# Kernel optimization log

Hardware: AMD Instinct MI355X
Metric: run time of the kernel (lower is better)

Reference implementation:

```python
import jax, jax.numpy as jnp
import numpy as np

B, M, V, E, D, T = 512, 64, 20000, 1024, 384, 100
EPS = 1e-5


def setup_inputs() -> dict:
    key = jax.random.key(0)
    ks = jax.random.split(key, 26)
    w = lambda k, shape: (jax.random.normal(k, shape, jnp.float32) * 0.02)
    return {
        'x': jax.random.uniform(ks[0], (B, V), jnp.float32),
        'emb': jax.random.normal(ks[1], (B, M, D), jnp.float32),
        'lengths': jax.random.randint(ks[2], (B,), 1, M + 1, jnp.int32),
        'fc11_w': w(ks[3], (E, V)), 'fc11_b': jnp.zeros((E,), jnp.float32),
        'fc12_w': w(ks[4], (E, E)), 'fc12_b': jnp.zeros((E,), jnp.float32),
        'q_w': w(ks[5], (D, E)), 'q_b': jnp.zeros((D,), jnp.float32),
        'k_w': w(ks[6], (D, D)), 'k_b': jnp.zeros((D,), jnp.float32),
        'v_w': w(ks[7], (D, D)), 'v_b': jnp.zeros((D,), jnp.float32),
        'mean_w': w(ks[8], (T, D)), 'mean_b': jnp.zeros((T,), jnp.float32),
        'logvar_w': w(ks[9], (T, D)), 'logvar_b': jnp.zeros((T,), jnp.float32),
        'mean_bn_b': jnp.zeros((T,), jnp.float32),
        'logvar_bn_b': jnp.zeros((T,), jnp.float32),
        'dec_w': w(ks[10], (V, T)), 'dec_b': jnp.zeros((V,), jnp.float32),
        'dec_bn_b': jnp.zeros((V,), jnp.float32),
    }


def _bn(h, bias):
    # BatchNorm1d, training-mode batch stats, weight frozen at 1 (requires_grad=False)
    mu = h.mean(axis=0)
    var = h.var(axis=0)  # biased variance, as torch BN normalization
    return (h - mu) / jnp.sqrt(var + EPS) + bias


def reference(x, emb, lengths, fc11_w, fc11_b, fc12_w, fc12_b,
              q_w, q_b, k_w, k_b, v_w, v_b,
              mean_w, mean_b, logvar_w, logvar_b,
              mean_bn_b, logvar_bn_b, dec_w, dec_b, dec_bn_b):
    # encoder MLP (dropout p=0 -> identity)
    e1 = jax.nn.softplus(x @ fc11_w.T + fc11_b)
    h_bow = jax.nn.softplus(e1 @ fc12_w.T + fc12_b)  # [B, E]

    # ragged single-query attention over sentence embeddings, vectorized
    q = h_bow @ q_w.T + q_b                              # [B, D]
    k = jnp.einsum('bmd,ed->bme', emb, k_w) + k_b        # [B, M, D]
    v = jnp.einsum('bmd,ed->bme', emb, v_w) + v_b        # [B, M, D]
    scores = jnp.einsum('bd,bmd->bm', q, k) / jnp.sqrt(jnp.float32(D))
    valid = jnp.arange(M)[None, :] < lengths[:, None]    # [B, M]
    scores = jnp.where(valid, scores, -jnp.inf)
    alpha = jax.nn.softmax(scores, axis=-1)
    d_i = jnp.einsum('bm,bmd->bd', alpha, v)             # [B, D]

    mu = _bn(d_i @ mean_w.T + mean_b, mean_bn_b)         # [B, T]
    logvar = _bn(d_i @ logvar_w.T + logvar_b, logvar_bn_b)
    z = mu  # eval-mode reparameterize
    theta = jax.nn.softmax(z, axis=1)

    logit = theta @ dec_w.T + dec_b
    recon_log = jax.nn.log_softmax(_bn(logit, dec_bn_b), axis=-1)
    recon_loss = -(x * recon_log).sum(axis=1).mean()

    # KL prior: a = ones -> mu2 = 0, var2 = 1 - 1/T (scalar)
    var2 = 1.0 - 1.0 / T
    var = jnp.exp(logvar)
    kld = 0.5 * ((var / var2 + mu * mu / var2 + jnp.log(var2) - logvar).sum(axis=1) - T)
    loss_kl = kld.mean()
    return recon_loss + loss_kl
```

## Files before the change

kernel.cpp:

```cpp
#include <hip/hip_runtime.h>
#include <cstddef>

#define NB 512
#define NM 64
#define NV 20000
#define NE 1024
#define ND 384
#define NT 100
#define EPS 1e-5f

#define NVP 20096
#define NKP 128
#define NHS 256

typedef __bf16 bf16x8 __attribute__((ext_vector_type(8)));
typedef float f32x4 __attribute__((ext_vector_type(4)));

__device__ __forceinline__ float softplus_f(float x) {
    return fmaxf(x, 0.f) + log1pf(expf(-fabsf(x)));
}

__device__ __forceinline__ unsigned short f2bf(float f) {
    unsigned u = __builtin_bit_cast(unsigned, f);
    unsigned r = u + 0x7FFFu + ((u >> 16) & 1u);
    return (unsigned short)(r >> 16);
}

__device__ __forceinline__ float bf2f(unsigned short u) {
    return __builtin_bit_cast(float, (unsigned)u << 16);
}

__device__ __forceinline__ uint4 pack_bf8(float4 a, float4 b) {
    bf16x8 v;
    v[0] = (__bf16)a.x; v[1] = (__bf16)a.y; v[2] = (__bf16)a.z; v[3] = (__bf16)a.w;
    v[4] = (__bf16)b.x; v[5] = (__bf16)b.y; v[6] = (__bf16)b.z; v[7] = (__bf16)b.w;
    return __builtin_bit_cast(uint4, v);
}

__device__ __forceinline__ void convert8(const float* __restrict__ s,
                                         unsigned short* __restrict__ d,
                                         int b, int tid) {
    const size_t i = ((size_t)b * 256 + tid) * 8;
    const float4 a = *reinterpret_cast<const float4*>(s + i);
    const float4 c = *reinterpret_cast<const float4*>(s + i + 4);
    *reinterpret_cast<uint4*>(d + i) = pack_bf8(a, c);
}

#define PREP_C12 512
#define PREP_QW  192
#define PREP_VW  72
#define PREP_TR  144
#define PREP_HD  257
#define PREP_DW  (NVP / 2)
#define PREP_BLOCKS (PREP_C12 + PREP_QW + PREP_VW + PREP_TR + PREP_HD + PREP_DW)

__global__ __launch_bounds__(256) void prep_kernel(
        const float* __restrict__ fc12_w, unsigned short* __restrict__ w12b,
        const float* __restrict__ q_w,    unsigned short* __restrict__ qwb,
        const float* __restrict__ v_w,    unsigned short* __restrict__ vwb,
        const float* __restrict__ k_w,    unsigned short* __restrict__ kTb,
        const float* __restrict__ mw, const float* __restrict__ lw,
        const float* __restrict__ mb, const float* __restrict__ lb,
        unsigned short* __restrict__ headwb, float* __restrict__ headbb,
        const float* __restrict__ dec_w,  unsigned short* __restrict__ decwb) {
    __shared__ float tile[32][33];
    int b = blockIdx.x;
    const int tid = threadIdx.x;
    if (b < PREP_C12) { convert8(fc12_w, w12b, b, tid); return; }
    b -= PREP_C12;
    if (b < PREP_QW) { convert8(q_w, qwb, b, tid); return; }
    b -= PREP_QW;
    if (b < PREP_VW) { convert8(v_w, vwb, b, tid); return; }
    b -= PREP_VW;
    if (b < PREP_TR) {
        const int bx = (b % 12) * 32, by = (b / 12) * 32;
        const int tx = tid & 31, ty = tid >> 5;
        #pragma unroll
        for (int i = 0; i < 4; ++i)
            tile[ty + 8 * i][tx] = k_w[(size_t)(by + ty + 8 * i) * ND + bx + tx];
        __syncthreads();
        #pragma unroll
        for (int i = 0; i < 4; ++i)
            kTb[(size_t)(bx + ty + 8 * i) * ND + by + tx] = f2bf(tile[tx][ty + 8 * i]);
        return;
    }
    b -= PREP_TR;
    if (b < PREP_HD) {
        if (b == NHS) {
            if (tid < NHS)
                headbb[tid] = (tid < NT) ? mb[tid]
                            : (tid >= 128 && tid < 128 + NT) ? lb[tid - 128] : 0.f;
            return;
        }
        const float* src = (b < NT) ? (mw + (size_t)b * ND)
                         : (b >= 128 && b < 128 + NT) ? (lw + (size_t)(b - 128) * ND) : nullptr;
        for (int c = tid; c < ND; c += 256)
            headwb[(size_t)b * ND + c] = src ? f2bf(src[c]) : (unsigned short)0;
        return;
    }
    b -= PREP_HD;
    {
        const int n = b * 2 + (tid >> 7);
        const int k = tid & 127;
        decwb[(size_t)n * NKP + k] =
            (n < NV && k < NT) ? f2bf(dec_w[(size_t)n * NT + k]) : (unsigned short)0;
    }
}

#define BM 128
#define BN 128
#define BK 32

__device__ __forceinline__ int lds_off(int row, int slot) {
    return row * BK + ((slot ^ ((row >> 1) & 3)) << 3);
}

__global__ __launch_bounds__(512, 2) void gemm_f32_256(
        const float* __restrict__ A,
        const float* __restrict__ Bw,
        unsigned short* __restrict__ partial,
        int M, int N, int K, int S, int steps_total) {
    __shared__ __align__(16) unsigned short Asl[256 * BK];
    __shared__ __align__(16) unsigned short Bsl[256 * BK];
    const int tid = threadIdx.x;
    const int xcd = blockIdx.x & 7;
    const int l = blockIdx.x >> 3;
    const int tile = l & 7;
    const int s = xcd + 8 * (l >> 3);
    const int bm = tile & 1, bn = tile >> 1;
    const int row0 = bm * 256, col0 = bn * 256;
    const int k_begin = (int)(((long)s * steps_total) / S) * BK;
    const int k_end   = (int)(((long)(s + 1) * steps_total) / S) * BK;
    const int nsteps = (k_end - k_begin) / BK;

    const int sr = tid >> 1;
    const int sc = (tid & 1) * 16;
    const int sslot = (tid & 1) * 2;
    const int wave = tid >> 6, lane = tid & 63;
    const int wm = wave >> 2, wn = wave & 3;
    const int lrow = lane & 15, lkb = lane >> 4;

    f32x4 acc[8][4] = {};
    const float* Ab = A + (size_t)row0 * K;
    const float* Bb = Bw + (size_t)col0 * K;

    float4 ra[4], rb[4];

#define LOADREGS(K0)                                                          \
    {                                                                         \
        const float* pa = Ab + (size_t)sr * K + (K0) + sc;                    \
        const float* pb = Bb + (size_t)sr * K + (K0) + sc;                    \
        ra[0] = *reinterpret_cast<const float4*>(pa);                         \
        ra[1] = *reinterpret_cast<const float4*>(pa + 4);                     \
        ra[2] = *reinterpret_cast<const float4*>(pa + 8);                     \
        ra[3] = *reinterpret_cast<const float4*>(pa + 12);                    \
        rb[0] = *reinterpret_cast<const float4*>(pb);                         \
        rb[1] = *reinterpret_cast<const float4*>(pb + 4);                     \
        rb[2] = *reinterpret_cast<const float4*>(pb + 8);                     \
        rb[3] = *reinterpret_cast<const float4*>(pb + 12);                    \
    }

#define WRITELDS()                                                            \
    {                                                                         \
        *reinterpret_cast<uint4*>(&Asl[lds_off(sr, sslot)])     = pack_bf8(ra[0], ra[1]); \
        *reinterpret_cast<uint4*>(&Asl[lds_off(sr, sslot + 1)]) = pack_bf8(ra[2], ra[3]); \
        *reinterpret_cast<uint4*>(&Bsl[lds_off(sr, sslot)])     = pack_bf8(rb[0], rb[1]); \
        *reinterpret_cast<uint4*>(&Bsl[lds_off(sr, sslot + 1)]) = pack_bf8(rb[2], rb[3]); \
    }

    LOADREGS(k_begin);
    WRITELDS();
    __syncthreads();

    for (int t = 0; t < nsteps; ++t) {
        const bool has_next = (t + 1) < nsteps;
        if (has_next) LOADREGS(k_begin + (t + 1) * BK);

        bf16x8 af[8], bfr[4];
        #pragma unroll
        for (int i = 0; i < 8; ++i)
            af[i] = *reinterpret_cast<const bf16x8*>(&Asl[lds_off(wm * 128 + i * 16 + lrow, lkb)]);
        #pragma unroll
        for (int j = 0; j < 4; ++j)
            bfr[j] = *reinterpret_cast<const bf16x8*>(&Bsl[lds_off(wn * 64 + j * 16 + lrow, lkb)]);
        #pragma unroll
        for (int i = 0; i < 8; ++i)
            #pragma unroll
            for (int j = 0; j < 4; ++j)
                acc[i][j] = __builtin_amdgcn_mfma_f32_16x16x32_bf16(af[i], bfr[j], acc[i][j], 0, 0, 0);

        __syncthreads();
        if (has_next) WRITELDS();
        __syncthreads();
    }
#undef LOADREGS
#undef WRITELDS

    unsigned short* P = partial + (size_t)s * M * N;
    #pragma unroll
    for (int i = 0; i < 8; ++i) {
        const int rbase = row0 + wm * 128 + i * 16 + lkb * 4;
        #pragma unroll
        for (int j = 0; j < 4; ++j) {
            const int col = col0 + wn * 64 + j * 16 + lrow;
            #pragma unroll
            for (int r = 0; r < 4; ++r)
                P[(size_t)(rbase + r) * N + col] = f2bf(acc[i][j][r]);
        }
    }
}

__global__ __launch_bounds__(256) void gemm_mfma_splitk(
        const unsigned short* __restrict__ A,
        const unsigned short* __restrict__ Bw,
        unsigned short* __restrict__ partial,
        int M, int N, int K, int S, int steps_total) {
    __shared__ __align__(16) unsigned short Asl[BM * BK];
    __shared__ __align__(16) unsigned short Bsl[BN * BK];
    const int tid = threadIdx.x;
    const int bn = blockIdx.x, bm = blockIdx.y, s = blockIdx.z;
    const int row0 = bm * BM, col0 = bn * BN;
    const int k_begin = (int)(((long)s * steps_total) / S) * BK;
    const int k_end   = (int)(((long)(s + 1) * steps_total) / S) * BK;

    const int srow = tid >> 2;
    const int scol = (tid & 3) * 8;
    const int wave = tid >> 6, lane = tid & 63;
    const int wm = wave >> 1, wn = wave & 1;
    const int lrow = lane & 15, lkb = lane >> 4;

    f32x4 acc[4][4] = {};
    const unsigned short* Ab = A + (size_t)row0 * K;
    const unsigned short* Bb = Bw + (size_t)col0 * K;

    for (int k0 = k_begin; k0 < k_end; k0 += BK) {
        #pragma unroll
        for (int i = 0; i < 2; ++i) {
            const int r = i * 64 + srow;
            __builtin_amdgcn_global_load_lds(
                (const __attribute__((address_space(1))) void*)(Ab + (size_t)r * K + k0 + scol),
                (__attribute__((address_space(3))) void*)(&Asl[(i * 256 + tid) * 8]),
                16, 0, 0);
            __builtin_amdgcn_global_load_lds(
                (const __attribute__((address_space(1))) void*)(Bb + (size_t)r * K + k0 + scol),
                (__attribute__((address_space(3))) void*)(&Bsl[(i * 256 + tid) * 8]),
                16, 0, 0);
        }
        __syncthreads();
        bf16x8 af[4], bfr[4];
        #pragma unroll
        for (int i = 0; i < 4; ++i) {
            af[i]  = *reinterpret_cast<const bf16x8*>(&Asl[(wm * 64 + i * 16 + lrow) * BK + lkb * 8]);
            bfr[i] = *reinterpret_cast<const bf16x8*>(&Bsl[(wn * 64 + i * 16 + lrow) * BK + lkb * 8]);
        }
        #pragma unroll
        for (int i = 0; i < 4; ++i)
            #pragma unroll
            for (int j = 0; j < 4; ++j)
                acc[i][j] = __builtin_amdgcn_mfma_f32_16x16x32_bf16(af[i], bfr[j], acc[i][j], 0, 0, 0);
        __syncthreads();
    }

    unsigned short* P = partial + (size_t)s * M * N;
    #pragma unroll
    for (int i = 0; i < 4; ++i) {
        const int rbase = row0 + wm * 64 + i * 16 + lkb * 4;
        #pragma unroll
        for (int j = 0; j < 4; ++j) {
            const int col = col0 + wn * 64 + j * 16 + lrow;
            #pragma unroll
            for (int r = 0; r < 4; ++r)
                P[(size_t)(rbase + r) * N + col] = f2bf(acc[i][j][r]);
        }
    }
}

__global__ __launch_bounds__(256) void gemm64_splitk(
        const unsigned short* __restrict__ A,
        const unsigned short* __restrict__ Bw,
        unsigned short* __restrict__ partial,
        int M, int N, int K, int S, int steps_total) {
    __shared__ __align__(16) unsigned short Asl[64 * BK];
    __shared__ __align__(16) unsigned short Bsl[64 * BK];
    const int tid = threadIdx.x;
    const int bn = blockIdx.x, bm = blockIdx.y, s = blockIdx.z;
    const int row0 = bm * 64, col0 = bn * 64;
    const int k_begin = (int)(((long)s * steps_total) / S) * BK;
    const int k_end   = (int)(((long)(s + 1) * steps_total) / S) * BK;

    const int srow = tid >> 2;
    const int scol = (tid & 3) * 8;
    const int wave = tid >> 6, lane = tid & 63;
    const int wm = wave >> 1, wn = wave & 1;
    const int lrow = lane & 15, lkb = lane >> 4;

    f32x4 acc[2][2] = {};
    const unsigned short* Ab = A + (size_t)row0 * K;
    const unsigned short* Bb = Bw + (size_t)col0 * K;

    for (int k0 = k_begin; k0 < k_end; k0 += BK) {
        __builtin_amdgcn_global_load_lds(
            (const __attribute__((address_space(1))) void*)(Ab + (size_t)srow * K + k0 + scol),
            (__attribute__((address_space(3))) void*)(&Asl[tid * 8]),
            16, 0, 0);
        __builtin_amdgcn_global_load_lds(
            (const __attribute__((address_space(1))) void*)(Bb + (size_t)srow * K + k0 + scol),
            (__attribute__((address_space(3))) void*)(&Bsl[tid * 8]),
            16, 0, 0);
        __syncthreads();
        bf16x8 af[2], bfr[2];
        #pragma unroll
        for (int i = 0; i < 2; ++i) {
            af[i]  = *reinterpret_cast<const bf16x8*>(&Asl[(wm * 32 + i * 16 + lrow) * BK + lkb * 8]);
            bfr[i] = *reinterpret_cast<const bf16x8*>(&Bsl[(wn * 32 + i * 16 + lrow) * BK + lkb * 8]);
        }
        #pragma unroll
        for (int i = 0; i < 2; ++i)
            #pragma unroll
            for (int j = 0; j < 2; ++j)
                acc[i][j] = __builtin_amdgcn_mfma_f32_16x16x32_bf16(af[i], bfr[j], acc[i][j], 0, 0, 0);
        __syncthreads();
    }

    unsigned short* P = partial + (size_t)s * M * N;
    #pragma unroll
    for (int i = 0; i < 2; ++i) {
        const int rbase = row0 + wm * 32 + i * 16 + lkb * 4;
        #pragma unroll
        for (int j = 0; j < 2; ++j) {
            const int col = col0 + wn * 32 + j * 16 + lrow;
            #pragma unroll
            for (int r = 0; r < 4; ++r)
                P[(size_t)(rbase + r) * N + col] = f2bf(acc[i][j][r]);
        }
    }
}

template<int OUT_BF16, int ACT, int HASBIAS>
__global__ __launch_bounds__(256) void reduce_splitk_bf(
        const unsigned short* __restrict__ partial,
        const float* __restrict__ bias,
        void* __restrict__ out, int MN, int N, int S) {
    const int i0 = (blockIdx.x * 256 + threadIdx.x) * 8;
    if (i0 >= MN) return;
    float sum[8] = {};
    for (int s = 0; s < S; ++s) {
        union { uint4 v; unsigned short u[8]; } p;
        p.v = *reinterpret_cast<const uint4*>(partial + (size_t)s * MN + i0);
        #pragma unroll
        for (int j = 0; j < 8; ++j) sum[j] += bf2f(p.u[j]);
    }
    if (HASBIAS) {
        const int nb = i0 % N;
        #pragma unroll
        for (int j = 0; j < 8; ++j) sum[j] += bias[nb + j];
    }
    if (ACT) {
        #pragma unroll
        for (int j = 0; j < 8; ++j) sum[j] = softplus_f(sum[j]);
    }
    if (OUT_BF16) {
        union { uint4 v; unsigned short u[8]; } r;
        #pragma unroll
        for (int j = 0; j < 8; ++j) r.u[j] = f2bf(sum[j]);
        *reinterpret_cast<uint4*>((unsigned short*)out + i0) = r.v;
    } else {
        float* o = (float*)out + i0;
        *reinterpret_cast<float4*>(o)     = make_float4(sum[0], sum[1], sum[2], sum[3]);
        *reinterpret_cast<float4*>(o + 4) = make_float4(sum[4], sum[5], sum[6], sum[7]);
    }
}

template<int OUT_BF16, int ACT, int HASBIAS, int COLSTATS>
__global__ __launch_bounds__(256) void gemm_mfma(
        const unsigned short* __restrict__ A,
        const unsigned short* __restrict__ Bw,
        const float* __restrict__ bias,
        void* __restrict__ Cout,
        float* __restrict__ colp,
        int M, int Nout, int K) {
    __shared__ __align__(16) unsigned short Asl[BM * BK];
    __shared__ __align__(16) unsigned short Bsl[BN * BK];
    const int tid = threadIdx.x;
    const int row0 = blockIdx.y * BM, col0 = blockIdx.x * BN;
    const int srow = tid >> 2;
    const int scol = (tid & 3) * 8;
    const int wave = tid >> 6, lane = tid & 63;
    const int wm = wave >> 1, wn = wave & 1;
    const int lrow = lane & 15, lkb = lane >> 4;

    f32x4 acc[4][4] = {};
    const unsigned short* Ab = A + (size_t)row0 * K;
    const unsigned short* Bb = Bw + (size_t)col0 * K;

    for (int k0 = 0; k0 < K; k0 += BK) {
        #pragma unroll
        for (int i = 0; i < 2; ++i) {
            const int r = i * 64 + srow;
            __builtin_amdgcn_global_load_lds(
                (const __attribute__((address_space(1))) void*)(Ab + (size_t)r * K + k0 + scol),
                (__attribute__((address_space(3))) void*)(&Asl[(i * 256 + tid) * 8]),
                16, 0, 0);
            __builtin_amdgcn_global_load_lds(
                (const __attribute__((address_space(1))) void*)(Bb + (size_t)r * K + k0 + scol),
                (__attribute__((address_space(3))) void*)(&Bsl[(i * 256 + tid) * 8]),
                16, 0, 0);
        }
        __syncthreads();
        bf16x8 af[4], bfr[4];
        #pragma unroll
        for (int i = 0; i < 4; ++i) {
            af[i]  = *reinterpret_cast<const bf16x8*>(&Asl[(wm * 64 + i * 16 + lrow) * BK + lkb * 8]);
            bfr[i] = *reinterpret_cast<const bf16x8*>(&Bsl[(wn * 64 + i * 16 + lrow) * BK + lkb * 8]);
        }
        #pragma unroll
        for (int i = 0; i < 4; ++i)
            #pragma unroll
            for (int j = 0; j < 4; ++j)
                acc[i][j] = __builtin_amdgcn_mfma_f32_16x16x32_bf16(af[i], bfr[j], acc[i][j], 0, 0, 0);
        __syncthreads();
    }

    #pragma unroll
    for (int j = 0; j < 4; ++j) {
        const int col = col0 + wn * 64 + j * 16 + lrow;
        const bool cok = col < Nout;
        const float bv = HASBIAS ? (cok ? bias[col] : 0.f) : 0.f;
        float csum = 0.f, csq = 0.f;
        #pragma unroll
        for (int i = 0; i < 4; ++i) {
            const int rbase = row0 + wm * 64 + i * 16 + lkb * 4;
            #pragma unroll
            for (int r = 0; r < 4; ++r) {
                float v = acc[i][j][r] + bv;
                if (ACT == 1) v = softplus_f(v);
                if (COLSTATS) { csum += v; csq = fmaf(v, v, csq); }
                if (cok) {
                    if (OUT_BF16)
                        ((unsigned short*)Cout)[(size_t)(rbase + r) * Nout + col] = f2bf(v);
                    else
                        ((float*)Cout)[(size_t)(rbase + r) * Nout + col] = v;
                }
            }
        }
        if (COLSTATS) {
            csum += __shfl_xor(csum, 16); csum += __shfl_xor(csum, 32);
            csq  += __shfl_xor(csq, 16);  csq  += __shfl_xor(csq, 32);
            if (lkb == 0) {
                const int w8 = blockIdx.y * 2 + wm;
                colp[(size_t)w8 * NVP + col] = csum;
                colp[(size_t)(8 + w8) * NVP + col] = csq;
            }
        }
    }
}

__global__ __launch_bounds__(256) void attn_kernel(const unsigned short* __restrict__ qkp,
                                                   const float* __restrict__ emb,
                                                   const int* __restrict__ lengths,
                                                   unsigned short* __restrict__ cb) {
    const int b = blockIdx.x;
    const int tid = threadIdx.x;
    __shared__ unsigned short es[NM * ND];
    __shared__ float qs[ND];
    __shared__ float sc[NM];

    const float* ebase = emb + (size_t)b * NM * ND;
    for (int i = tid; i < NM * ND / 8; i += 256) {
        const float4 v0 = *reinterpret_cast<const float4*>(ebase + (size_t)i * 8);
        const float4 v1 = *reinterpret_cast<const float4*>(ebase + (size_t)i * 8 + 4);
        *reinterpret_cast<uint4*>(&es[i * 8]) = pack_bf8(v0, v1);
    }
    for (int d = tid; d < ND; d += 256) {
        float acc = 0.f;
        #pragma unroll
        for (int s = 0; s < 8; ++s)
            acc += bf2f(qkp[((size_t)s * NB + b) * ND + d]);
        qs[d] = acc;
    }
    __syncthreads();

    const int wave = tid >> 6, lane = tid & 63;
    const float scale = 0.05103103630798288f;

    for (int m = wave; m < NM; m += 4) {
        float s = 0.f;
        for (int d = lane; d < ND; d += 64) s = fmaf(bf2f(es[m * ND + d]), qs[d], s);
        #pragma unroll
        for (int off = 32; off; off >>= 1) s += __shfl_xor(s, off);
        if (lane == 0) sc[m] = s * scale;
    }
    __syncthreads();

    const int len = lengths[b];
    if (tid < 64) {
        float s = (tid < len) ? sc[tid] : -INFINITY;
        float mx = s;
        #pragma unroll
        for (int off = 32; off; off >>= 1) mx = fmaxf(mx, __shfl_xor(mx, off));
        float e = (tid < len) ? expf(s - mx) : 0.f;
        float sum = e;
        #pragma unroll
        for (int off = 32; off; off >>= 1) sum += __shfl_xor(sum, off);
        sc[tid] = e / sum;
    }
    __syncthreads();

    for (int d = tid; d < ND; d += 256) {
        float acc = 0.f;
        for (int m = 0; m < len; ++m) acc = fmaf(sc[m], bf2f(es[m * ND + d]), acc);
        cb[(size_t)b * ND + d] = f2bf(acc);
    }
}

__global__ __launch_bounds__(256) void bn_batch(const float* __restrict__ hl,
                                                const float* __restrict__ mbnb,
                                                const float* __restrict__ lbnb,
                                                float* __restrict__ mu,
                                                float* __restrict__ lv) {
    const int t = blockIdx.x;
    const int sel = blockIdx.y;
    const int col = sel ? 128 + t : t;
    const float* bnb = sel ? lbnb : mbnb;
    float* dst = sel ? lv : mu;
    const int tid = threadIdx.x;

    float s = 0.f, ss = 0.f;
    for (int b = tid; b < NB; b += 256) {
        const float v = hl[(size_t)b * NHS + col];
        s += v; ss += v * v;
    }
    __shared__ float rs[256], rss[256];
    rs[tid] = s; rss[tid] = ss;
    __syncthreads();
    for (int off = 128; off; off >>= 1) {
        if (tid < off) { rs[tid] += rs[tid + off]; rss[tid] += rss[tid + off]; }
        __syncthreads();
    }
    const float mean = rs[0] / (float)NB;
    const float var = rss[0] / (float)NB - mean * mean;
    const float rstd = rsqrtf(var + EPS);
    const float bb = bnb[t];
    for (int b = tid; b < NB; b += 256) {
        dst[(size_t)b * NT + t] = (hl[(size_t)b * NHS + col] - mean) * rstd + bb;
    }
}

__global__ __launch_bounds__(128) void theta_kl(const float* __restrict__ mu,
                                                const float* __restrict__ lv,
                                                unsigned short* __restrict__ thetab,
                                                float* __restrict__ kld_p) {
    const int b = blockIdx.x, tid = threadIdx.x;
    const float var2 = 1.0f - 1.0f / (float)NT;
    const float inv_var2 = 1.0f / var2;
    __shared__ float red[128];

    const float m = (tid < NT) ? mu[(size_t)b * NT + tid] : -INFINITY;
    red[tid] = m;
    __syncthreads();
    for (int off = 64; off; off >>= 1) {
        if (tid < off) red[tid] = fmaxf(red[tid], red[tid + off]);
        __syncthreads();
    }
    const float mx = red[0];
    __syncthreads();

    const float e = (tid < NT) ? expf(m - mx) : 0.f;
    red[tid] = e;
    __syncthreads();
    for (int off = 64; off; off >>= 1) {
        if (tid < off) red[tid] += red[tid + off];
        __syncthreads();
    }
    const float sum = red[0];
    __syncthreads();
    thetab[(size_t)b * NKP + tid] = (tid < NT) ? f2bf(e / sum) : (unsigned short)0;

    float term = 0.f;
    if (tid < NT) {
        const float l = lv[(size_t)b * NT + tid];
        term = expf(l) * inv_var2 + m * m * inv_var2 - l;
    }
    red[tid] = term;
    __syncthreads();
    for (int off = 64; off; off >>= 1) {
        if (tid < off) red[tid] += red[tid + off];
        __syncthreads();
    }
    if (tid == 0)
        kld_p[b] = 0.5f * (red[0] + (float)NT * logf(var2) - (float)NT);
}

__global__ __launch_bounds__(256) void stats_final(const float* __restrict__ colp,
                                                   float* __restrict__ cmu,
                                                   float* __restrict__ crstd) {
    const int v = blockIdx.x * 256 + threadIdx.x;
    if (v >= NV) return;
    float s = 0.f, q = 0.f;
    #pragma unroll
    for (int w = 0; w < 8; ++w) {
        s += colp[(size_t)w * NVP + v];
        q += colp[(size_t)(8 + w) * NVP + v];
    }
    const float mean = s / (float)NB;
    cmu[v] = mean;
    crstd[v] = rsqrtf(q / (float)NB - mean * mean + EPS);
}

__global__ __launch_bounds__(256) void row_recon(const unsigned short* __restrict__ logitb,
                                                 const float* __restrict__ x,
                                                 const float* __restrict__ cmu,
                                                 const float* __restrict__ crstd,
                                                 const float* __restrict__ dbnb,
                                                 float* __restrict__ recon_p) {
    const int b = blockIdx.x, tid = threadIdx.x;
    const unsigned short* lr = logitb + (size_t)b * NV;
    const float* xr = x + (size_t)b * NV;

    float m_i = -INFINITY, s_i = 0.f, xz = 0.f, xs = 0.f;
    for (int v = tid * 8; v < NV; v += 2048) {
        union { uint4 v4; unsigned short u[8]; } lw;
        lw.v4 = *reinterpret_cast<const uint4*>(lr + v);
        const float4 x0 = *reinterpret_cast<const float4*>(xr + v);
        const float4 x1 = *reinterpret_cast<const float4*>(xr + v + 4);
        const float4 c0 = *reinterpret_cast<const float4*>(cmu + v);
        const float4 c1 = *reinterpret_cast<const float4*>(cmu + v + 4);
        const float4 r0 = *reinterpret_cast<const float4*>(crstd + v);
        const float4 r1 = *reinterpret_cast<const float4*>(crstd + v + 4);
        const float4 d0 = *reinterpret_cast<const float4*>(dbnb + v);
        const float4 d1 = *reinterpret_cast<const float4*>(dbnb + v + 4);
        const float xv[8] = {x0.x,x0.y,x0.z,x0.w,x1.x,x1.y,x1.z,x1.w};
        const float cm[8] = {c0.x,c0.y,c0.z,c0.w,c1.x,c1.y,c1.z,c1.w};
        const float cr[8] = {r0.x,r0.y,r0.z,r0.w,r1.x,r1.y,r1.z,r1.w};
        const float db[8] = {d0.x,d0.y,d0.z,d0.w,d1.x,d1.y,d1.z,d1.w};
        float z[8];
        #pragma unroll
        for (int j = 0; j < 8; ++j)
            z[j] = fmaf(bf2f(lw.u[j]) - cm[j], cr[j], db[j]);
        float mx = z[0];
        #pragma unroll
        for (int j = 1; j < 8; ++j) mx = fmaxf(mx, z[j]);
        const float mnew = fmaxf(m_i, mx);
        float e8 = 0.f;
        #pragma unroll
        for (int j = 0; j < 8; ++j) e8 += expf(z[j] - mnew);
        s_i = s_i * expf(m_i - mnew) + e8;
        m_i = mnew;
        #pragma unroll
        for (int j = 0; j < 8; ++j) {
            xz = fmaf(xv[j], z[j], xz);
            xs += xv[j];
        }
    }

    __shared__ float rm[256], rs[256], rxz[256], rxs[256];
    rm[tid] = m_i; rs[tid] = s_i; rxz[tid] = xz; rxs[tid] = xs;
    __syncthreads();
    for (int off = 128; off; off >>= 1) {
        if (tid < off) {
            const float m1 = rm[tid], m2 = rm[tid + off];
            const float s1 = rs[tid], s2 = rs[tid + off];
            const float mm = fmaxf(m1, m2);
            rm[tid] = mm;
            rs[tid] = s1 * expf(m1 - mm) + s2 * expf(m2 - mm);
            rxz[tid] += rxz[tid + off];
            rxs[tid] += rxs[tid + off];
        }
        __syncthreads();
    }
    if (tid == 0) {
        const float lse = rm[0] + logf(rs[0]);
        recon_p[b] = rxz[0] - lse * rxs[0];
    }
}

__global__ __launch_bounds__(512) void finalize(const float* __restrict__ recon_p,
                                                const float* __restrict__ kld_p,
                                                float* __restrict__ out) {
    const int tid = threadIdx.x;
    __shared__ float r1[512], r2[512];
    r1[tid] = recon_p[tid];
    r2[tid] = kld_p[tid];
    __syncthreads();
    for (int off = 256; off; off >>= 1) {
        if (tid < off) { r1[tid] += r1[tid + off]; r2[tid] += r2[tid + off]; }
        __syncthreads();
    }
    if (tid == 0) out[0] = (-r1[0] + r2[0]) / (float)NB;
}

extern "C" void kernel_launch(void* const* d_in, const int* in_sizes, int n_in,
                              void* d_out, int out_size, void* d_ws, size_t ws_size,
                              hipStream_t stream) {
    const float* x       = (const float*)d_in[0];
    const float* emb     = (const float*)d_in[1];
    const int*   lengths = (const int*)d_in[2];
    const float* fc11_w  = (const float*)d_in[3];
    const float* fc11_b  = (const float*)d_in[4];
    const float* fc12_w  = (const float*)d_in[5];
    const float* fc12_b  = (const float*)d_in[6];
    const float* q_w     = (const float*)d_in[7];
    const float* q_b     = (const float*)d_in[8];
    const float* k_w     = (const float*)d_in[9];
    const float* v_w     = (const float*)d_in[11];
    const float* v_b     = (const float*)d_in[12];
    const float* mean_w  = (const float*)d_in[13];
    const float* mean_b  = (const float*)d_in[14];
    const float* lvw     = (const float*)d_in[15];
    const float* lvb     = (const float*)d_in[16];
    const float* mbnb    = (const float*)d_in[17];
    const float* lbnb    = (const float*)d_in[18];
    const float* dec_w   = (const float*)d_in[19];
    const float* dec_b   = (const float*)d_in[20];
    const float* dbnb    = (const float*)d_in[21];
    float* out = (float*)d_out;

    char* base = (char*)d_ws;
    size_t off = 0;
    auto alloc = [&](size_t bytes) -> void* {
        void* p = base + off;
        off += (bytes + 255) & ~(size_t)255;
        return p;
    };

    unsigned short* w12b   = (unsigned short*)alloc((size_t)NE * NE * 2);
    unsigned short* e1b    = (unsigned short*)alloc((size_t)NB * NE * 2);
    unsigned short* hb     = (unsigned short*)alloc((size_t)NB * NE * 2);
    unsigned short* qwb    = (unsigned short*)alloc((size_t)ND * NE * 2);
    unsigned short* kTb    = (unsigned short*)alloc((size_t)ND * ND * 2);
    unsigned short* vwb    = (unsigned short*)alloc((size_t)ND * ND * 2);
    unsigned short* qb     = (unsigned short*)alloc((size_t)NB * ND * 2);
    unsigned short* cb     = (unsigned short*)alloc((size_t)NB * ND * 2);
    unsigned short* dib    = (unsigned short*)alloc((size_t)NB * ND * 2);
    unsigned short* headwb = (unsigned short*)alloc((size_t)NHS * ND * 2);
    float*          headbb = (float*)alloc((size_t)NHS * 4);
    float*          hl     = (float*)alloc((size_t)NB * NHS * 4);
    float*          mu     = (float*)alloc((size_t)NB * NT * 4);
    float*          lv     = (float*)alloc((size_t)NB * NT * 4);
    float*          colp   = (float*)alloc((size_t)16 * NVP * 4);
    float*          cmu    = (float*)alloc((size_t)NV * 4);
    float*          crstd  = (float*)alloc((size_t)NV * 4);
    float*          rp     = (float*)alloc((size_t)NB * 4);
    float*          kp     = (float*)alloc((size_t)NB * 4);
    unsigned short* decwb  = (unsigned short*)alloc((size_t)NVP * NKP * 2);
    unsigned short* thetab = (unsigned short*)alloc((size_t)NB * NKP * 2);
    unsigned short* smallp = (unsigned short*)alloc((size_t)16 * NB * ND * 2);
    const size_t part_per_s = (size_t)NB * NE * 2;
    const size_t logit_bytes = (size_t)NB * NV * 2;
    const size_t remain = (ws_size > off) ? (ws_size - off) : 0;
    const int S11 = (remain >= 32 * part_per_s) ? 32
                  : (remain >= 16 * part_per_s + logit_bytes) ? 16 : 8;
    size_t part_alloc = S11 * part_per_s;
    if (part_alloc < logit_bytes) part_alloc = logit_bytes;
    unsigned short* partb = (unsigned short*)alloc(part_alloc);
    unsigned short* logitb = partb;

    const dim3 blk(256);

    prep_kernel<<<PREP_BLOCKS, blk, 0, stream>>>(
        fc12_w, w12b, q_w, qwb, v_w, vwb, k_w, kTb,
        mean_w, lvw, mean_b, lvb, headwb, headbb, dec_w, decwb);

    gemm_f32_256<<<8 * S11, 512, 0, stream>>>(
        x, fc11_w, partb, NB, NE, NV, S11, NV / BK);
    reduce_splitk_bf<1, 1, 1><<<(NB * NE) / 2048, blk, 0, stream>>>(
        partb, fc11_b, e1b, NB * NE, NE, S11);

    gemm_mfma_splitk<<<dim3(NE / BN, NB / BM, 8), blk, 0, stream>>>(
        e1b, w12b, partb, NB, NE, NE, 8, NE / BK);
    reduce_splitk_bf<1, 1, 1><<<(NB * NE) / 2048, blk, 0, stream>>>(
        partb, fc12_b, hb, NB * NE, NE, 8);

    gemm64_splitk<<<dim3(ND / 64, NB / 64, 16), blk, 0, stream>>>(
        hb, qwb, smallp, NB, ND, NE, 16, NE / BK);
    reduce_splitk_bf<1, 0, 1><<<(NB * ND) / 2048, blk, 0, stream>>>(
        smallp, q_b, qb, NB * ND, ND, 16);
    gemm64_splitk<<<dim3(ND / 64, NB / 64, 8), blk, 0, stream>>>(
        qb, kTb, smallp, NB, ND, ND, 8, ND / BK);
    attn_kernel<<<NB, 256, 0, stream>>>(smallp, emb, lengths, cb);
    gemm64_splitk<<<dim3(ND / 64, NB / 64, 8), blk, 0, stream>>>(
        cb, vwb, smallp, NB, ND, ND, 8, ND / BK);
    reduce_splitk_bf<1, 0, 1><<<(NB * ND) / 2048, blk, 0, stream>>>(
        smallp, v_b, dib, NB * ND, ND, 8);
    gemm64_splitk<<<dim3(NHS / 64, NB / 64, 8), blk, 0, stream>>>(
        dib, headwb, smallp, NB, NHS, ND, 8, ND / BK);
    reduce_splitk_bf<0, 0, 1><<<(NB * NHS) / 2048, blk, 0, stream>>>(
        smallp, headbb, hl, NB * NHS, NHS, 8);
    bn_batch<<<dim3(NT, 2), blk, 0, stream>>>(hl, mbnb, lbnb, mu, lv);
    theta_kl<<<NB, 128, 0, stream>>>(mu, lv, thetab, kp);
    gemm_mfma<1, 0, 1, 1><<<dim3(NVP / BN, NB / BM), blk, 0, stream>>>(
        thetab, decwb, dec_b, logitb, colp, NB, NV, NKP);
    stats_final<<<(NV + 255) / 256, blk, 0, stream>>>(colp, cmu, crstd);
    row_recon<<<NB, 256, 0, stream>>>(logitb, x, cmu, crstd, dbnb, rp);
    finalize<<<1, 512, 0, stream>>>(rp, kp, out);
}
```

Before: 167.5 us.

## Shrink fc11 GEMM tiles to 128x128 with LDS padding and vectorize dec_w prep

```diff
diff --git a/kernel.cpp b/kernel.cpp
--- a/kernel.cpp
+++ b/kernel.cpp
@@ -51,7 +51,7 @@
 #define PREP_VW  72
 #define PREP_TR  144
 #define PREP_HD  257
-#define PREP_DW  (NVP / 2)
+#define PREP_DW  (NVP / 16)
 #define PREP_BLOCKS (PREP_C12 + PREP_QW + PREP_VW + PREP_TR + PREP_HD + PREP_DW)
 
 __global__ __launch_bounds__(256) void prep_kernel(
@@ -100,10 +100,15 @@
     }
     b -= PREP_HD;
     {
-        const int n = b * 2 + (tid >> 7);
-        const int k = tid & 127;
-        decwb[(size_t)n * NKP + k] =
-            (n < NV && k < NT) ? f2bf(dec_w[(size_t)n * NT + k]) : (unsigned short)0;
+        const int n = b * 16 + (tid >> 4);
+        const int k0 = (tid & 15) * 8;
+        union { unsigned short u[8]; uint4 v; } r;
+        #pragma unroll
+        for (int jj = 0; jj < 8; ++jj) {
+            const int k = k0 + jj;
+            r.u[jj] = (n < NV && k < NT) ? f2bf(dec_w[(size_t)n * NT + k]) : (unsigned short)0;
+        }
+        *reinterpret_cast<uint4*>(&decwb[(size_t)n * NKP + k0]) = r.v;
     }
 }
 
@@ -111,40 +116,41 @@
 #define BN 128
 #define BK 32
 
-__device__ __forceinline__ int lds_off(int row, int slot) {
-    return row * BK + ((slot ^ ((row >> 1) & 3)) << 3);
-}
-
-__global__ __launch_bounds__(512, 2) void gemm_f32_256(
+__device__ __forceinline__ int lds_off128(int row, int slot) {
+    return row * BK + ((slot ^ (row & 3)) << 3);
+}
+
+__global__ __launch_bounds__(512) void gemm_f32_128(
         const float* __restrict__ A,
         const float* __restrict__ Bw,
         unsigned short* __restrict__ partial,
         int M, int N, int K, int S, int steps_total) {
-    __shared__ __align__(16) unsigned short Asl[256 * BK];
-    __shared__ __align__(16) unsigned short Bsl[256 * BK];
+    __shared__ __align__(16) unsigned short ldspool[49152];
+    unsigned short* Asl = ldspool;
+    unsigned short* Bsl = ldspool + BM * BK;
     const int tid = threadIdx.x;
     const int xcd = blockIdx.x & 7;
-    const int l = blockIdx.x >> 3;
-    const int tile = l & 7;
-    const int s = xcd + 8 * (l >> 3);
-    const int bm = tile & 1, bn = tile >> 1;
-    const int row0 = bm * 256, col0 = bn * 256;
+    const int j = blockIdx.x >> 3;
+    const int tile = j & 31;
+    const int s = xcd + 8 * (j >> 5);
+    const int bm = tile & 3, bn = tile >> 2;
+    const int row0 = bm * BM, col0 = bn * BN;
     const int k_begin = (int)(((long)s * steps_total) / S) * BK;
     const int k_end   = (int)(((long)(s + 1) * steps_total) / S) * BK;
     const int nsteps = (k_end - k_begin) / BK;
 
-    const int sr = tid >> 1;
-    const int sc = (tid & 1) * 16;
-    const int sslot = (tid & 1) * 2;
+    const int sr = tid >> 2;
+    const int sc = (tid & 3) * 8;
+    const int sslot = tid & 3;
     const int wave = tid >> 6, lane = tid & 63;
     const int wm = wave >> 2, wn = wave & 3;
     const int lrow = lane & 15, lkb = lane >> 4;
 
-    f32x4 acc[8][4] = {};
+    f32x4 acc[4][2] = {};
     const float* Ab = A + (size_t)row0 * K;
     const float* Bb = Bw + (size_t)col0 * K;
 
-    float4 ra[4], rb[4];
+    float4 ra[2], rb[2];
 
 #define LOADREGS(K0)                                                          \
     {                                                                         \
@@ -152,20 +158,14 @@
         const float* pb = Bb + (size_t)sr * K + (K0) + sc;                    \
         ra[0] = *reinterpret_cast<const float4*>(pa);                         \
         ra[1] = *reinterpret_cast<const float4*>(pa + 4);                     \
-        ra[2] = *reinterpret_cast<const float4*>(pa + 8);                     \
-        ra[3] = *reinterpret_cast<const float4*>(pa + 12);                    \
         rb[0] = *reinterpret_cast<const float4*>(pb);                         \
         rb[1] = *reinterpret_cast<const float4*>(pb + 4);                     \
-        rb[2] = *reinterpret_cast<const float4*>(pb + 8);                     \
-        rb[3] = *reinterpret_cast<const float4*>(pb + 12);                    \
     }
 
 #define WRITELDS()                                                            \
     {                                                                         \
-        *reinterpret_cast<uint4*>(&Asl[lds_off(sr, sslot)])     = pack_bf8(ra[0], ra[1]); \
-        *reinterpret_cast<uint4*>(&Asl[lds_off(sr, sslot + 1)]) = pack_bf8(ra[2], ra[3]); \
-        *reinterpret_cast<uint4*>(&Bsl[lds_off(sr, sslot)])     = pack_bf8(rb[0], rb[1]); \
-        *reinterpret_cast<uint4*>(&Bsl[lds_off(sr, sslot + 1)]) = pack_bf8(rb[2], rb[3]); \
+        *reinterpret_cast<uint4*>(&Asl[lds_off128(sr, sslot)]) = pack_bf8(ra[0], ra[1]); \
+        *reinterpret_cast<uint4*>(&Bsl[lds_off128(sr, sslot)]) = pack_bf8(rb[0], rb[1]); \
     }
 
     LOADREGS(k_begin);
@@ -176,18 +176,18 @@
         const bool has_next = (t + 1) < nsteps;
         if (has_next) LOADREGS(k_begin + (t + 1) * BK);
 
-        bf16x8 af[8], bfr[4];
-        #pragma unroll
-        for (int i = 0; i < 8; ++i)
-            af[i] = *reinterpret_cast<const bf16x8*>(&Asl[lds_off(wm * 128 + i * 16 + lrow, lkb)]);
-        #pragma unroll
-        for (int j = 0; j < 4; ++j)
-            bfr[j] = *reinterpret_cast<const bf16x8*>(&Bsl[lds_off(wn * 64 + j * 16 + lrow, lkb)]);
-        #pragma unroll
-        for (int i = 0; i < 8; ++i)
+        bf16x8 af[4], bfr[2];
+        #pragma unroll
+        for (int i = 0; i < 4; ++i)
+            af[i] = *reinterpret_cast<const bf16x8*>(&Asl[lds_off128(wm * 64 + i * 16 + lrow, lkb)]);
+        #pragma unroll
+        for (int j2 = 0; j2 < 2; ++j2)
+            bfr[j2] = *reinterpret_cast<const bf16x8*>(&Bsl[lds_off128(wn * 32 + j2 * 16 + lrow, lkb)]);
+        #pragma unroll
+        for (int i = 0; i < 4; ++i)
             #pragma unroll
-            for (int j = 0; j < 4; ++j)
-                acc[i][j] = __builtin_amdgcn_mfma_f32_16x16x32_bf16(af[i], bfr[j], acc[i][j], 0, 0, 0);
+            for (int j2 = 0; j2 < 2; ++j2)
+                acc[i][j2] = __builtin_amdgcn_mfma_f32_16x16x32_bf16(af[i], bfr[j2], acc[i][j2], 0, 0, 0);
 
         __syncthreads();
         if (has_next) WRITELDS();
@@ -198,14 +198,15 @@
 
     unsigned short* P = partial + (size_t)s * M * N;
     #pragma unroll
-    for (int i = 0; i < 8; ++i) {
-        const int rbase = row0 + wm * 128 + i * 16 + lkb * 4;
-        #pragma unroll
-        for (int j = 0; j < 4; ++j) {
-            const int col = col0 + wn * 64 + j * 16 + lrow;
+    for (int i = 0; i < 4; ++i) {
+        const int rbase = row0 + wm * 64 + i * 16 + lkb * 4;
+        #pragma unroll
+        for (int j2 = 0; j2 < 2; ++j2) {
+            const int col = col0 + wn * 32 + j2 * 16 + lrow;
             #pragma unroll
             for (int r = 0; r < 4; ++r)
-                P[(size_t)(rbase + r) * N + col] = f2bf(acc[i][j][r]);
+                __builtin_nontemporal_store(f2bf(acc[i][j2][r]),
+                                            &P[(size_t)(rbase + r) * N + col]);
         }
     }
 }
@@ -761,7 +762,7 @@
         fc12_w, w12b, q_w, qwb, v_w, vwb, k_w, kTb,
         mean_w, lvw, mean_b, lvb, headwb, headbb, dec_w, decwb);
 
-    gemm_f32_256<<<8 * S11, 512, 0, stream>>>(
+    gemm_f32_128<<<32 * S11, 512, 0, stream>>>(
         x, fc11_w, partb, NB, NE, NV, S11, NV / BK);
     reduce_splitk_bf<1, 1, 1><<<(NB * NE) / 2048, blk, 0, stream>>>(
         partb, fc11_b, e1b, NB * NE, NE, S11);
```

Result: slower. 197.4 us (+17.9%).

## Double-buffer global prefetch registers in split-K GEMM and vectorize dec_w prep

Applied to the files above, without the earlier changes.

```diff
diff --git a/kernel.cpp b/kernel.cpp
--- a/kernel.cpp
+++ b/kernel.cpp
@@ -51,7 +51,7 @@
 #define PREP_VW  72
 #define PREP_TR  144
 #define PREP_HD  257
-#define PREP_DW  (NVP / 2)
+#define PREP_DW  (NVP / 16)
 #define PREP_BLOCKS (PREP_C12 + PREP_QW + PREP_VW + PREP_TR + PREP_HD + PREP_DW)
 
 __global__ __launch_bounds__(256) void prep_kernel(
@@ -100,10 +100,15 @@
     }
     b -= PREP_HD;
     {
-        const int n = b * 2 + (tid >> 7);
-        const int k = tid & 127;
-        decwb[(size_t)n * NKP + k] =
-            (n < NV && k < NT) ? f2bf(dec_w[(size_t)n * NT + k]) : (unsigned short)0;
+        const int n = b * 16 + (tid >> 4);
+        const int k0 = (tid & 15) * 8;
+        union { unsigned short u[8]; uint4 v; } r;
+        #pragma unroll
+        for (int jj = 0; jj < 8; ++jj) {
+            const int k = k0 + jj;
+            r.u[jj] = (n < NV && k < NT) ? f2bf(dec_w[(size_t)n * NT + k]) : (unsigned short)0;
+        }
+        *reinterpret_cast<uint4*>(&decwb[(size_t)n * NKP + k0]) = r.v;
     }
 }
 
@@ -144,37 +149,41 @@
     const float* Ab = A + (size_t)row0 * K;
     const float* Bb = Bw + (size_t)col0 * K;
 
-    float4 ra[4], rb[4];
-
-#define LOADREGS(K0)                                                          \
+    float4 ra0[4], rb0[4], ra1[4], rb1[4];
+
+#define LOADREGS(RA, RB, K0)                                                  \
     {                                                                         \
         const float* pa = Ab + (size_t)sr * K + (K0) + sc;                    \
         const float* pb = Bb + (size_t)sr * K + (K0) + sc;                    \
-        ra[0] = *reinterpret_cast<const float4*>(pa);                         \
-        ra[1] = *reinterpret_cast<const float4*>(pa + 4);                     \
-        ra[2] = *reinterpret_cast<const float4*>(pa + 8);                     \
-        ra[3] = *reinterpret_cast<const float4*>(pa + 12);                    \
-        rb[0] = *reinterpret_cast<const float4*>(pb);                         \
-        rb[1] = *reinterpret_cast<const float4*>(pb + 4);                     \
-        rb[2] = *reinterpret_cast<const float4*>(pb + 8);                     \
-        rb[3] = *reinterpret_cast<const float4*>(pb + 12);                    \
-    }
-
-#define WRITELDS()                                                            \
+        RA[0] = *reinterpret_cast<const float4*>(pa);                         \
+        RA[1] = *reinterpret_cast<const float4*>(pa + 4);                     \
+        RA[2] = *reinterpret_cast<const float4*>(pa + 8);                     \
+        RA[3] = *reinterpret_cast<const float4*>(pa + 12);                    \
+        RB[0] = *reinterpret_cast<const float4*>(pb);                         \
+        RB[1] = *reinterpret_cast<const float4*>(pb + 4);                     \
+        RB[2] = *reinterpret_cast<const float4*>(pb + 8);                     \
+        RB[3] = *reinterpret_cast<const float4*>(pb + 12);                    \
+    }
+
+#define WRITELDS(RA, RB)                                                      \
     {                                                                         \
-        *reinterpret_cast<uint4*>(&Asl[lds_off(sr, sslot)])     = pack_bf8(ra[0], ra[1]); \
-        *reinterpret_cast<uint4*>(&Asl[lds_off(sr, sslot + 1)]) = pack_bf8(ra[2], ra[3]); \
-        *reinterpret_cast<uint4*>(&Bsl[lds_off(sr, sslot)])     = pack_bf8(rb[0], rb[1]); \
-        *reinterpret_cast<uint4*>(&Bsl[lds_off(sr, sslot + 1)]) = pack_bf8(rb[2], rb[3]); \
-    }
-
-    LOADREGS(k_begin);
-    WRITELDS();
+        *reinterpret_cast<uint4*>(&Asl[lds_off(sr, sslot)])     = pack_bf8(RA[0], RA[1]); \
+        *reinterpret_cast<uint4*>(&Asl[lds_off(sr, sslot + 1)]) = pack_bf8(RA[2], RA[3]); \
+        *reinterpret_cast<uint4*>(&Bsl[lds_off(sr, sslot)])     = pack_bf8(RB[0], RB[1]); \
+        *reinterpret_cast<uint4*>(&Bsl[lds_off(sr, sslot + 1)]) = pack_bf8(RB[2], RB[3]); \
+    }
+
+    LOADREGS(ra0, rb0, k_begin);
+    WRITELDS(ra0, rb0);
+    if (nsteps > 1) LOADREGS(ra1, rb1, k_begin + BK);
     __syncthreads();
 
     for (int t = 0; t < nsteps; ++t) {
-        const bool has_next = (t + 1) < nsteps;
-        if (has_next) LOADREGS(k_begin + (t + 1) * BK);
+        const bool even = (t & 1) == 0;
+        if (t + 2 < nsteps) {
+            if (even) LOADREGS(ra0, rb0, k_begin + (t + 2) * BK)
+            else      LOADREGS(ra1, rb1, k_begin + (t + 2) * BK)
+        }
 
         bf16x8 af[8], bfr[4];
         #pragma unroll
@@ -190,7 +199,10 @@
                 acc[i][j] = __builtin_amdgcn_mfma_f32_16x16x32_bf16(af[i], bfr[j], acc[i][j], 0, 0, 0);
 
         __syncthreads();
-        if (has_next) WRITELDS();
+        if (t + 1 < nsteps) {
+            if (even) WRITELDS(ra1, rb1)
+            else      WRITELDS(ra0, rb0)
+        }
         __syncthreads();
     }
 #undef LOADREGS
```

Result: slower. 181.2 us (+8.2%).
